# Optimization experiments

Hardware: AMD Instinct MI355X
Metric: run time of the kernel (lower is better)

## Reference

```python
import jax, jax.numpy as jnp
import numpy as np


def setup_inputs() -> dict:
    key = jax.random.key(0)
    k1, k2 = jax.random.split(key)
    N, B, E, H = 2048, 8, 256, 512
    x = jax.random.normal(k1, (N, B, E), dtype=jnp.float32)
    h = jax.random.normal(k2, (N, B, H), dtype=jnp.float32)
    return {"x": x, "h": h}


def reference(x, h):
    # x: (N, B, E), h: (N, B, H)
    H = h.shape[-1]
    xt = jnp.transpose(x, (1, 0, 2))            # (B, N, E)
    norm = jnp.linalg.norm(xt, axis=2, keepdims=True)  # (B, N, 1)
    xn = xt / norm
    # cosine-similarity scores, softmax over keys (last dim)
    scores = jax.nn.softmax(jnp.einsum('bie,bje->bij', xn, xn), axis=2)  # (B, N, N)
    ht = jnp.transpose(h, (1, 0, 2))            # (B, N, H)
    # The original expands scores/h over an H-fold dim, bmm's, and sums;
    # that equals H * (scores @ h). Keep the H factor for faithfulness
    # (it cancels in the global-norm division below).
    g = H * jnp.einsum('bij,bjh->bih', scores, ht)  # (B, N, H)
    g = jnp.transpose(g, (1, 0, 2))             # (N, B, H)
    return g / jnp.linalg.norm(g)
```

## Files before the change

kernel.cpp:

```cpp
#include <hip/hip_runtime.h>

#define N_TOK 2048
#define B_SZ  8
#define E_DIM 256
#define H_DIM 512
#define ITERS (N_TOK / 32)

typedef __attribute__((ext_vector_type(8))) short bf16x8;
typedef __attribute__((ext_vector_type(4))) float f32x4;
typedef __attribute__((ext_vector_type(4))) unsigned short u16x4;

__device__ __forceinline__ unsigned short f2bf(float f) {
    union { float f; unsigned u; } v; v.f = f;
    unsigned r = v.u + 0x7FFF + ((v.u >> 16) & 1);
    return (unsigned short)(r >> 16);
}
__device__ __forceinline__ float bf2f(unsigned short b) {
    union { unsigned u; float f; } v; v.u = ((unsigned)b) << 16;
    return v.f;
}

__global__ void prep_kernel(const float* __restrict__ x,
                            const float* __restrict__ hptr,
                            unsigned short* __restrict__ Xn,
                            unsigned short* __restrict__ Vp) {
    int bid = blockIdx.x;
    int t = threadIdx.x;
    if (bid < (N_TOK * B_SZ) / 4) {
        int w = t >> 6, lane = t & 63;
        int r = bid * 4 + w;
        int n = r >> 3, b = r & 7;
        float4 v = *(const float4*)(x + (size_t)r * E_DIM + lane * 4);
        float s = v.x * v.x + v.y * v.y + v.z * v.z + v.w * v.w;
        #pragma unroll
        for (int o = 32; o > 0; o >>= 1) s += __shfl_xor(s, o);
        float rn = 1.0f / sqrtf(s);
        u16x4 pk;
        pk[0] = f2bf(v.x * rn); pk[1] = f2bf(v.y * rn);
        pk[2] = f2bf(v.z * rn); pk[3] = f2bf(v.w * rn);
        int u = lane >> 1, half = lane & 1;
        *(u16x4*)(Xn + ((size_t)b * N_TOK + n) * E_DIM
                     + (size_t)((u ^ (n & 7)) * 8 + half * 4)) = pk;
    } else {
        int lin = bid - (N_TOK * B_SZ) / 4;
        int jb = lin & 63, hb = (lin >> 6) & 15, b = lin >> 10;
        __shared__ float tile[32][33];
        int j0 = jb * 32, h0 = hb * 32;
        int tx = t & 31, ty = t >> 5;
        #pragma unroll
        for (int it = 0; it < 4; it++) {
            int j = j0 + ty + it * 8;
            tile[ty + it * 8][tx] = hptr[((size_t)j * B_SZ + b) * H_DIM + h0 + tx];
        }
        __syncthreads();
        size_t base = ((size_t)b * (N_TOK / 32) + jb) * (H_DIM * 32);
        int hcl = t >> 3, jg = (t >> 1) & 3, half = t & 1;
        int hc = h0 + hcl;
        u16x4 pk;
        #pragma unroll
        for (int k = 0; k < 4; k++)
            pk[k] = f2bf(tile[jg * 8 + half * 4 + k][hcl]);
        *(u16x4*)(Vp + base + (size_t)(hc * 4 + (jg ^ ((hcl >> 1) & 3))) * 8
                     + half * 4) = pk;
    }
}

#define PT_STRIDE 40

__launch_bounds__(256, 2)
__global__ void flash_kernel(const unsigned short* __restrict__ Xn,
                             const unsigned short* __restrict__ Vp,
                             float* __restrict__ out,
                             float* __restrict__ sumsq) {
    __shared__ __attribute__((aligned(16))) unsigned short Kbuf[2][32 * 256];
    __shared__ __attribute__((aligned(16))) unsigned short Pt[2][16 * PT_STRIDE];
    __shared__ float Lred[2][2][16];

    int b  = blockIdx.x;
    int q0 = blockIdx.y * 32;
    int t = threadIdx.x;
    int w = t >> 6, lane = t & 63;
    int quad = lane >> 4, nm = lane & 15;
    int rg = w >> 1, kh = w & 1;

    const unsigned short* Kbase = Xn + (size_t)b * N_TOK * E_DIM;
    const unsigned short* Qrow =
        Xn + ((size_t)b * N_TOK + q0 + rg * 16 + nm) * E_DIM;
    const unsigned short* Vtile0 = Vp + (size_t)b * (N_TOK / 32) * (H_DIM * 32);

    bf16x8 qf[8];
    #pragma unroll
    for (int ec = 0; ec < 8; ec++)
        qf[ec] = *(const bf16x8*)(Qrow + (size_t)(((ec * 4 + quad) ^ (nm & 7)) * 8));

    f32x4 O[16];
    #pragma unroll
    for (int i = 0; i < 16; i++) O[i] = (f32x4){0.f, 0.f, 0.f, 0.f};
    float l_lane[4];
    #pragma unroll
    for (int r = 0; r < 4; r++) l_lane[r] = 0.0f;

    auto stage = [&](int tile, int buf) {
        const unsigned short* src0 = Kbase + (size_t)tile * 32 * E_DIM;
        #pragma unroll
        for (int k = 0; k < 4; k++) {
            int chunk = w * 4 + k;
            __builtin_amdgcn_global_load_lds(
                (const __attribute__((address_space(1))) unsigned int*)
                    (src0 + (size_t)chunk * 512 + lane * 8),
                (__attribute__((address_space(3))) unsigned int*)
                    (&Kbuf[buf][chunk * 512]),
                16, 0, 0);
        }
    };

    stage(0, 0);
    int vswz = (quad ^ ((nm >> 1) & 3)) * 8;
    int krow = kh * 16 + nm;

    for (int it = 0; it < ITERS; ++it) {
        __syncthreads();
        int cur = it & 1;

        const unsigned short* Vt = Vtile0 + (size_t)it * (H_DIM * 32);
        bf16x8 vf[16];
        #pragma unroll
        for (int tt = 0; tt < 16; tt++) {
            int hc = kh * 256 + tt * 16 + nm;
            vf[tt] = *(const bf16x8*)(Vt + (size_t)(hc * 4) * 8 + vswz);
        }

        if (it + 1 < ITERS) stage(it + 1, cur ^ 1);
        const unsigned short* KB = &Kbuf[cur][0];

        f32x4 sa = (f32x4){0.f,0.f,0.f,0.f}, sb = (f32x4){0.f,0.f,0.f,0.f};
        #pragma unroll
        for (int ec = 0; ec < 4; ec++) {
            int u0 = (((2*ec)   * 4 + quad) ^ (nm & 7)) * 8;
            int u1 = (((2*ec+1) * 4 + quad) ^ (nm & 7)) * 8;
            bf16x8 kf0 = *(const bf16x8*)(KB + krow * 256 + u0);
            bf16x8 kf1 = *(const bf16x8*)(KB + krow * 256 + u1);
            sa = __builtin_amdgcn_mfma_f32_16x16x32_bf16(qf[2*ec],   kf0, sa, 0, 0, 0);
            sb = __builtin_amdgcn_mfma_f32_16x16x32_bf16(qf[2*ec+1], kf1, sb, 0, 0, 0);
        }

        #pragma unroll
        for (int r = 0; r < 4; r++) {
            unsigned short pb = f2bf(__expf((sa[r] + sb[r]) - 1.0f));
            l_lane[r] += bf2f(pb);
            Pt[rg][(quad * 4 + r) * PT_STRIDE + kh * 16 + nm] = pb;
        }

        asm volatile("s_waitcnt lgkmcnt(0)" ::: "memory");
        __builtin_amdgcn_s_barrier();
        asm volatile("" ::: "memory");

        bf16x8 pf = *(const bf16x8*)(&Pt[rg][nm * PT_STRIDE + quad * 8]);

        #pragma unroll
        for (int tt = 0; tt < 16; tt++)
            O[tt] = __builtin_amdgcn_mfma_f32_16x16x32_bf16(pf, vf[tt], O[tt], 0, 0, 0);
    }

    float lv[4];
    #pragma unroll
    for (int r = 0; r < 4; r++) {
        float v = l_lane[r];
        #pragma unroll
        for (int o = 1; o < 16; o <<= 1) v += __shfl_xor(v, o);
        lv[r] = v;
    }
    if (nm == 0) {
        #pragma unroll
        for (int r = 0; r < 4; r++) Lred[rg][kh][quad * 4 + r] = lv[r];
    }
    __syncthreads();
    float linv[4];
    #pragma unroll
    for (int r = 0; r < 4; r++)
        linv[r] = 1.0f / (Lred[rg][0][quad * 4 + r] + Lred[rg][1][quad * 4 + r]);

    float ss = 0.0f;
    #pragma unroll
    for (int tt = 0; tt < 16; tt++) {
        #pragma unroll
        for (int r = 0; r < 4; r++) {
            float val = O[tt][r] * linv[r];
            int row = q0 + rg * 16 + quad * 4 + r;
            int col = kh * 256 + tt * 16 + nm;
            out[((size_t)row * B_SZ + b) * H_DIM + col] = val;
            ss += val * val;
        }
    }
    #pragma unroll
    for (int o = 1; o < 64; o <<= 1) ss += __shfl_xor(ss, o);
    if (lane == 0) atomicAdd(sumsq, ss);
}

__global__ void scale_kernel(float* __restrict__ out,
                             const float* __restrict__ sumsq) {
    size_t idx = ((size_t)blockIdx.x * blockDim.x + threadIdx.x) * 4;
    float rs = 1.0f / sqrtf(*sumsq);
    float4 v = *(float4*)(out + idx);
    v.x *= rs; v.y *= rs; v.z *= rs; v.w *= rs;
    *(float4*)(out + idx) = v;
}

extern "C" void kernel_launch(void* const* d_in, const int* in_sizes, int n_in,
                              void* d_out, int out_size, void* d_ws, size_t ws_size,
                              hipStream_t stream) {
    const float* x = (const float*)d_in[0];
    const float* h = (const float*)d_in[1];
    float* out = (float*)d_out;

    unsigned short* Xn = (unsigned short*)d_ws;
    unsigned short* Vp = Xn + (size_t)B_SZ * N_TOK * E_DIM;
    float* sumsq = (float*)(Vp + (size_t)B_SZ * N_TOK * H_DIM);

    hipMemsetAsync(sumsq, 0, sizeof(float), stream);
    prep_kernel<<<(N_TOK * B_SZ) / 4 + (N_TOK / 32) * (H_DIM / 32) * B_SZ,
                  256, 0, stream>>>(x, h, Xn, Vp);
    flash_kernel<<<dim3(B_SZ, N_TOK / 32), 256, 0, stream>>>(Xn, Vp, out, sumsq);
    scale_kernel<<<out_size / (4 * 256), 256, 0, stream>>>(out, sumsq);
}
```

Baseline: 223.2 us.

## Split key dimension across two blocks and combine partial outputs

The attention loop over keys is split into two halves, run as separate blocks along a new grid z dimension. Each block writes unnormalized partial outputs and row sums, and a new combine kernel adds them, normalizes and accumulates the global sum of squares. The goal is more parallelism: 1024 blocks instead of 512, with launch bounds raised to target higher occupancy. The cost is an extra full-size fp32 partial buffer written and read back, plus one more kernel launch. The memset is also folded into the prep kernel.

New measurement: 697.1 us. 3.12x slower.

```diff
diff --git a/kernel.cpp b/kernel.cpp
--- a/kernel.cpp
+++ b/kernel.cpp
@@ -4,7 +4,8 @@
 #define B_SZ  8
 #define E_DIM 256
 #define H_DIM 512
-#define ITERS (N_TOK / 32)
+#define KSPLIT 2
+#define TPB   (N_TOK / 32 / KSPLIT)
 
 typedef __attribute__((ext_vector_type(8))) short bf16x8;
 typedef __attribute__((ext_vector_type(4))) float f32x4;
@@ -23,9 +24,11 @@
 __global__ void prep_kernel(const float* __restrict__ x,
                             const float* __restrict__ hptr,
                             unsigned short* __restrict__ Xn,
-                            unsigned short* __restrict__ Vp) {
+                            unsigned short* __restrict__ Vp,
+                            float* __restrict__ sumsq) {
     int bid = blockIdx.x;
     int t = threadIdx.x;
+    if (bid == 0 && t == 0) *sumsq = 0.0f;
     if (bid < (N_TOK * B_SZ) / 4) {
         int w = t >> 6, lane = t & 63;
         int r = bid * 4 + w;
@@ -67,17 +70,19 @@
 
 #define PT_STRIDE 40
 
-__launch_bounds__(256, 2)
+__launch_bounds__(256, 4)
 __global__ void flash_kernel(const unsigned short* __restrict__ Xn,
                              const unsigned short* __restrict__ Vp,
-                             float* __restrict__ out,
-                             float* __restrict__ sumsq) {
+                             float* __restrict__ Op0,
+                             float* __restrict__ Op1,
+                             float* __restrict__ Lpart) {
     __shared__ __attribute__((aligned(16))) unsigned short Kbuf[2][32 * 256];
     __shared__ __attribute__((aligned(16))) unsigned short Pt[2][16 * PT_STRIDE];
     __shared__ float Lred[2][2][16];
 
     int b  = blockIdx.x;
     int q0 = blockIdx.y * 32;
+    int z  = blockIdx.z;
     int t = threadIdx.x;
     int w = t >> 6, lane = t & 63;
     int quad = lane >> 4, nm = lane & 15;
@@ -114,13 +119,15 @@
         }
     };
 
-    stage(0, 0);
+    int tile0 = z * TPB;
+    stage(tile0, 0);
     int vswz = (quad ^ ((nm >> 1) & 3)) * 8;
     int krow = kh * 16 + nm;
 
-    for (int it = 0; it < ITERS; ++it) {
+    for (int ii = 0; ii < TPB; ++ii) {
         __syncthreads();
-        int cur = it & 1;
+        int cur = ii & 1;
+        int it = tile0 + ii;
 
         const unsigned short* Vt = Vtile0 + (size_t)it * (H_DIM * 32);
         bf16x8 vf[16];
@@ -130,7 +137,7 @@
             vf[tt] = *(const bf16x8*)(Vt + (size_t)(hc * 4) * 8 + vswz);
         }
 
-        if (it + 1 < ITERS) stage(it + 1, cur ^ 1);
+        if (ii + 1 < TPB) stage(it + 1, cur ^ 1);
         const unsigned short* KB = &Kbuf[cur][0];
 
         f32x4 sa = (f32x4){0.f,0.f,0.f,0.f}, sb = (f32x4){0.f,0.f,0.f,0.f};
@@ -175,26 +182,50 @@
         for (int r = 0; r < 4; r++) Lred[rg][kh][quad * 4 + r] = lv[r];
     }
     __syncthreads();
-    float linv[4];
-    #pragma unroll
-    for (int r = 0; r < 4; r++)
-        linv[r] = 1.0f / (Lred[rg][0][quad * 4 + r] + Lred[rg][1][quad * 4 + r]);
-
-    float ss = 0.0f;
+    if (t < 32) {
+        int rgi = t >> 4, i = t & 15;
+        Lpart[(size_t)z * (N_TOK * B_SZ) + (size_t)(q0 + t) * B_SZ + b] =
+            Lred[rgi][0][i] + Lred[rgi][1][i];
+    }
+
+    float* Od = z ? Op1 : Op0;
     #pragma unroll
     for (int tt = 0; tt < 16; tt++) {
         #pragma unroll
         for (int r = 0; r < 4; r++) {
-            float val = O[tt][r] * linv[r];
             int row = q0 + rg * 16 + quad * 4 + r;
             int col = kh * 256 + tt * 16 + nm;
-            out[((size_t)row * B_SZ + b) * H_DIM + col] = val;
-            ss += val * val;
-        }
+            Od[((size_t)row * B_SZ + b) * H_DIM + col] = O[tt][r];
+        }
+    }
+}
+
+__global__ void combine_kernel(float* __restrict__ out,
+                               const float* __restrict__ Op1,
+                               const float* __restrict__ Lpart,
+                               float* __restrict__ sumsq) {
+    int t = threadIdx.x;
+    float ss = 0.0f;
+    #pragma unroll
+    for (int p = 0; p < 4; p++) {
+        size_t i4 = (size_t)blockIdx.x * 1024 + p * 256 + t;
+        size_t g = i4 * 4;
+        int r = (int)(g >> 9);
+        float linv = 1.0f / (Lpart[r] + Lpart[N_TOK * B_SZ + r]);
+        float4 a = *(const float4*)(out + g);
+        float4 c = *(const float4*)(Op1 + g);
+        float4 v;
+        v.x = (a.x + c.x) * linv; v.y = (a.y + c.y) * linv;
+        v.z = (a.z + c.z) * linv; v.w = (a.w + c.w) * linv;
+        *(float4*)(out + g) = v;
+        ss += v.x * v.x + v.y * v.y + v.z * v.z + v.w * v.w;
     }
     #pragma unroll
     for (int o = 1; o < 64; o <<= 1) ss += __shfl_xor(ss, o);
-    if (lane == 0) atomicAdd(sumsq, ss);
+    __shared__ float red[4];
+    if ((t & 63) == 0) red[t >> 6] = ss;
+    __syncthreads();
+    if (t == 0) atomicAdd(sumsq, red[0] + red[1] + red[2] + red[3]);
 }
 
 __global__ void scale_kernel(float* __restrict__ out,
@@ -215,11 +246,15 @@
 
     unsigned short* Xn = (unsigned short*)d_ws;
     unsigned short* Vp = Xn + (size_t)B_SZ * N_TOK * E_DIM;
-    float* sumsq = (float*)(Vp + (size_t)B_SZ * N_TOK * H_DIM);
-
-    hipMemsetAsync(sumsq, 0, sizeof(float), stream);
+    float* Op1 = (float*)(Vp + (size_t)B_SZ * N_TOK * H_DIM);
+    float* Lpart = Op1 + (size_t)N_TOK * B_SZ * H_DIM;
+    float* sumsq = Lpart + (size_t)KSPLIT * N_TOK * B_SZ;
+
     prep_kernel<<<(N_TOK * B_SZ) / 4 + (N_TOK / 32) * (H_DIM / 32) * B_SZ,
-                  256, 0, stream>>>(x, h, Xn, Vp);
-    flash_kernel<<<dim3(B_SZ, N_TOK / 32), 256, 0, stream>>>(Xn, Vp, out, sumsq);
+                  256, 0, stream>>>(x, h, Xn, Vp, sumsq);
+    flash_kernel<<<dim3(B_SZ, N_TOK / 32, KSPLIT), 256, 0, stream>>>(
+        Xn, Vp, out, Op1, Lpart);
+    combine_kernel<<<(N_TOK * B_SZ * H_DIM) / (256 * 16), 256, 0, stream>>>(
+        out, Op1, Lpart, sumsq);
     scale_kernel<<<out_size / (4 * 256), 256, 0, stream>>>(out, sumsq);
 }
```

## Split flash kernel across 8 waves with E-dim split and LDS score reduction

Applied to the files above, without the earlier changes.

Doubles the flash kernel block to 512 threads: the two score waves per key half each compute half of the E-dimension dot product, exchange partials through a new shared buffer, and one applies exp and writes P. Each wave now owns 128 output columns instead of 256, halving accumulator and V-fragment registers so more waves can be resident. The sumsq zeroing moves from a memset into prep_kernel, dropping one API call. In exchange there is an extra barrier per iteration and the exp work is done by only half the waves.

After: 244.1 us. +9.4%, slower.

```diff
diff --git a/kernel.cpp b/kernel.cpp
--- a/kernel.cpp
+++ b/kernel.cpp
@@ -23,9 +23,11 @@
 __global__ void prep_kernel(const float* __restrict__ x,
                             const float* __restrict__ hptr,
                             unsigned short* __restrict__ Xn,
-                            unsigned short* __restrict__ Vp) {
+                            unsigned short* __restrict__ Vp,
+                            float* __restrict__ sumsq) {
     int bid = blockIdx.x;
     int t = threadIdx.x;
+    if (bid == 0 && t == 0) *sumsq = 0.0f;
     if (bid < (N_TOK * B_SZ) / 4) {
         int w = t >> 6, lane = t & 63;
         int r = bid * 4 + w;
@@ -67,13 +69,14 @@
 
 #define PT_STRIDE 40
 
-__launch_bounds__(256, 2)
+__launch_bounds__(512, 4)
 __global__ void flash_kernel(const unsigned short* __restrict__ Xn,
                              const unsigned short* __restrict__ Vp,
                              float* __restrict__ out,
                              float* __restrict__ sumsq) {
     __shared__ __attribute__((aligned(16))) unsigned short Kbuf[2][32 * 256];
     __shared__ __attribute__((aligned(16))) unsigned short Pt[2][16 * PT_STRIDE];
+    __shared__ __attribute__((aligned(16))) float Spart[8][256];
     __shared__ float Lred[2][2][16];
 
     int b  = blockIdx.x;
@@ -81,21 +84,23 @@
     int t = threadIdx.x;
     int w = t >> 6, lane = t & 63;
     int quad = lane >> 4, nm = lane & 15;
-    int rg = w >> 1, kh = w & 1;
+    int es = w & 1, kh = (w >> 1) & 1, rg = w >> 2, pc = w & 3;
 
     const unsigned short* Kbase = Xn + (size_t)b * N_TOK * E_DIM;
     const unsigned short* Qrow =
         Xn + ((size_t)b * N_TOK + q0 + rg * 16 + nm) * E_DIM;
     const unsigned short* Vtile0 = Vp + (size_t)b * (N_TOK / 32) * (H_DIM * 32);
 
-    bf16x8 qf[8];
-    #pragma unroll
-    for (int ec = 0; ec < 8; ec++)
-        qf[ec] = *(const bf16x8*)(Qrow + (size_t)(((ec * 4 + quad) ^ (nm & 7)) * 8));
-
-    f32x4 O[16];
-    #pragma unroll
-    for (int i = 0; i < 16; i++) O[i] = (f32x4){0.f, 0.f, 0.f, 0.f};
+    bf16x8 qf[4];
+    #pragma unroll
+    for (int j = 0; j < 4; j++) {
+        int ec = es * 4 + j;
+        qf[j] = *(const bf16x8*)(Qrow + (size_t)(((ec * 4 + quad) ^ (nm & 7)) * 8));
+    }
+
+    f32x4 O[8];
+    #pragma unroll
+    for (int i = 0; i < 8; i++) O[i] = (f32x4){0.f, 0.f, 0.f, 0.f};
     float l_lane[4];
     #pragma unroll
     for (int r = 0; r < 4; r++) l_lane[r] = 0.0f;
@@ -103,8 +108,8 @@
     auto stage = [&](int tile, int buf) {
         const unsigned short* src0 = Kbase + (size_t)tile * 32 * E_DIM;
         #pragma unroll
-        for (int k = 0; k < 4; k++) {
-            int chunk = w * 4 + k;
+        for (int k = 0; k < 2; k++) {
+            int chunk = w * 2 + k;
             __builtin_amdgcn_global_load_lds(
                 (const __attribute__((address_space(1))) unsigned int*)
                     (src0 + (size_t)chunk * 512 + lane * 8),
@@ -123,56 +128,64 @@
         int cur = it & 1;
 
         const unsigned short* Vt = Vtile0 + (size_t)it * (H_DIM * 32);
-        bf16x8 vf[16];
-        #pragma unroll
-        for (int tt = 0; tt < 16; tt++) {
-            int hc = kh * 256 + tt * 16 + nm;
+        bf16x8 vf[8];
+        #pragma unroll
+        for (int tt = 0; tt < 8; tt++) {
+            int hc = pc * 128 + tt * 16 + nm;
             vf[tt] = *(const bf16x8*)(Vt + (size_t)(hc * 4) * 8 + vswz);
         }
 
         if (it + 1 < ITERS) stage(it + 1, cur ^ 1);
         const unsigned short* KB = &Kbuf[cur][0];
 
-        f32x4 sa = (f32x4){0.f,0.f,0.f,0.f}, sb = (f32x4){0.f,0.f,0.f,0.f};
-        #pragma unroll
-        for (int ec = 0; ec < 4; ec++) {
-            int u0 = (((2*ec)   * 4 + quad) ^ (nm & 7)) * 8;
-            int u1 = (((2*ec+1) * 4 + quad) ^ (nm & 7)) * 8;
-            bf16x8 kf0 = *(const bf16x8*)(KB + krow * 256 + u0);
-            bf16x8 kf1 = *(const bf16x8*)(KB + krow * 256 + u1);
-            sa = __builtin_amdgcn_mfma_f32_16x16x32_bf16(qf[2*ec],   kf0, sa, 0, 0, 0);
-            sb = __builtin_amdgcn_mfma_f32_16x16x32_bf16(qf[2*ec+1], kf1, sb, 0, 0, 0);
-        }
-
-        #pragma unroll
-        for (int r = 0; r < 4; r++) {
-            unsigned short pb = f2bf(__expf((sa[r] + sb[r]) - 1.0f));
-            l_lane[r] += bf2f(pb);
-            Pt[rg][(quad * 4 + r) * PT_STRIDE + kh * 16 + nm] = pb;
-        }
-
+        f32x4 s = (f32x4){0.f, 0.f, 0.f, 0.f};
+        #pragma unroll
+        for (int j = 0; j < 4; j++) {
+            int ec = es * 4 + j;
+            int u = ((ec * 4 + quad) ^ (nm & 7)) * 8;
+            bf16x8 kf = *(const bf16x8*)(KB + krow * 256 + u);
+            s = __builtin_amdgcn_mfma_f32_16x16x32_bf16(qf[j], kf, s, 0, 0, 0);
+        }
+
+        *(f32x4*)(&Spart[w][lane * 4]) = s;
         asm volatile("s_waitcnt lgkmcnt(0)" ::: "memory");
         __builtin_amdgcn_s_barrier();
         asm volatile("" ::: "memory");
 
+        if (es == 0) {
+            f32x4 s2 = *(const f32x4*)(&Spart[w ^ 1][lane * 4]);
+            #pragma unroll
+            for (int r = 0; r < 4; r++) {
+                unsigned short pb = f2bf(__expf((s[r] + s2[r]) - 1.0f));
+                l_lane[r] += bf2f(pb);
+                Pt[rg][(quad * 4 + r) * PT_STRIDE + kh * 16 + nm] = pb;
+            }
+        }
+
+        asm volatile("s_waitcnt lgkmcnt(0)" ::: "memory");
+        __builtin_amdgcn_s_barrier();
+        asm volatile("" ::: "memory");
+
         bf16x8 pf = *(const bf16x8*)(&Pt[rg][nm * PT_STRIDE + quad * 8]);
 
         #pragma unroll
-        for (int tt = 0; tt < 16; tt++)
+        for (int tt = 0; tt < 8; tt++)
             O[tt] = __builtin_amdgcn_mfma_f32_16x16x32_bf16(pf, vf[tt], O[tt], 0, 0, 0);
     }
 
-    float lv[4];
-    #pragma unroll
-    for (int r = 0; r < 4; r++) {
-        float v = l_lane[r];
-        #pragma unroll
-        for (int o = 1; o < 16; o <<= 1) v += __shfl_xor(v, o);
-        lv[r] = v;
-    }
-    if (nm == 0) {
-        #pragma unroll
-        for (int r = 0; r < 4; r++) Lred[rg][kh][quad * 4 + r] = lv[r];
+    if (es == 0) {
+        float lv[4];
+        #pragma unroll
+        for (int r = 0; r < 4; r++) {
+            float v = l_lane[r];
+            #pragma unroll
+            for (int o = 1; o < 16; o <<= 1) v += __shfl_xor(v, o);
+            lv[r] = v;
+        }
+        if (nm == 0) {
+            #pragma unroll
+            for (int r = 0; r < 4; r++) Lred[rg][kh][quad * 4 + r] = lv[r];
+        }
     }
     __syncthreads();
     float linv[4];
@@ -182,12 +195,12 @@
 
     float ss = 0.0f;
     #pragma unroll
-    for (int tt = 0; tt < 16; tt++) {
+    for (int tt = 0; tt < 8; tt++) {
         #pragma unroll
         for (int r = 0; r < 4; r++) {
             float val = O[tt][r] * linv[r];
             int row = q0 + rg * 16 + quad * 4 + r;
-            int col = kh * 256 + tt * 16 + nm;
+            int col = pc * 128 + tt * 16 + nm;
             out[((size_t)row * B_SZ + b) * H_DIM + col] = val;
             ss += val * val;
         }
@@ -217,9 +230,8 @@
     unsigned short* Vp = Xn + (size_t)B_SZ * N_TOK * E_DIM;
     float* sumsq = (float*)(Vp + (size_t)B_SZ * N_TOK * H_DIM);
 
-    hipMemsetAsync(sumsq, 0, sizeof(float), stream);
     prep_kernel<<<(N_TOK * B_SZ) / 4 + (N_TOK / 32) * (H_DIM / 32) * B_SZ,
-                  256, 0, stream>>>(x, h, Xn, Vp);
-    flash_kernel<<<dim3(B_SZ, N_TOK / 32), 256, 0, stream>>>(Xn, Vp, out, sumsq);
+                  256, 0, stream>>>(x, h, Xn, Vp, sumsq);
+    flash_kernel<<<dim3(B_SZ, N_TOK / 32), 512, 0, stream>>>(Xn, Vp, out, sumsq);
     scale_kernel<<<out_size / (4 * 256), 256, 0, stream>>>(out, sumsq);
 }
```
